# Kernel optimization log

Hardware: AMD Instinct MI355X
Metric: run time of the kernel (lower is better)

## Reference

```python
import jax, jax.numpy as jnp
import numpy as np

B, T, C, H, N = 2, 1024, 2048, 32, 64  # C == H*N, head_size fixed at 64
LAYER, NLAYERS = 12, 24
EPS = 1e-5 * 64.0  # GroupNorm eps = 1e-5 * 8**2


def _structured_params():
    r01 = LAYER / (NLAYERS - 1)          # ratio_0_to_1
    r1a0 = 1.0 - LAYER / NLAYERS         # ratio_1_to_almost0
    ddd = np.arange(C, dtype=np.float64) / C
    n = np.arange(C, dtype=np.float64)
    p = {}
    p['maa_x'] = 1.0 - ddd ** r1a0
    p['maa_w'] = 1.0 - ddd ** r1a0
    p['maa_k'] = 1.0 - ddd ** r1a0
    p['maa_v'] = 1.0 - (ddd ** r1a0 + 0.3 * r01)
    p['maa_r'] = 1.0 - ddd ** (0.5 * r1a0)
    p['maa_g'] = 1.0 - ddd ** (0.5 * r1a0)
    p['time_decay'] = -6.0 + 5.0 * (n / (C - 1)) ** (0.7 + 1.3 * r01)
    zig = ((n + 1) % 3 - 1) * 0.1
    p['u'] = (r01 * (1.0 - n / (C - 1)) + zig).reshape(H, N)  # time_faaaa
    return {k: jnp.asarray(v, jnp.float32) for k, v in p.items()}


def setup_inputs():
    key = jax.random.key(0)
    ks = jax.random.split(key, 12)
    inp = {'x': jax.random.normal(ks[0], (B, T, C), jnp.float32)}
    inp.update(_structured_params())
    inp['maa_w1'] = jax.random.uniform(ks[1], (C, 5 * 32), jnp.float32, -1e-4, 1e-4)
    inp['maa_w2'] = jax.random.uniform(ks[2], (5, 32, C), jnp.float32, -1e-4, 1e-4)
    inp['td_w1'] = jax.random.uniform(ks[3], (C, 64), jnp.float32, -1e-4, 1e-4)
    inp['td_w2'] = jax.random.uniform(ks[4], (64, C), jnp.float32, -1e-4, 1e-4)
    for i, name in enumerate(['Wr', 'Wk', 'Wv', 'Wg', 'Wo']):
        inp[name] = jax.random.normal(ks[5 + i], (C, C), jnp.float32) * 0.02  # applied as x @ W
    inp['ln_g'] = jnp.ones((C,), jnp.float32)
    inp['ln_b'] = jnp.zeros((C,), jnp.float32)
    return inp


def _wkv6(r, k, v, w, u):
    # r,k,v,w: [B,T,C]; u: [H,N].  y_t = r_t . (u*k_t v_t^T + S_t); S_{t+1} = exp(-exp(w_t))*S_t + k_t v_t^T
    def heads(a):
        return a.reshape(B, T, H, N).transpose(1, 0, 2, 3)  # [T,B,H,N]
    r, k, v = heads(r), heads(k), heads(v)
    d = jnp.exp(-jnp.exp(heads(w)))  # data-dependent per-channel decay

    def step(S, inp):
        r_t, k_t, v_t, d_t = inp  # each [B,H,N]
        y = jnp.einsum('bhj,bhji->bhi', r_t, S) \
            + jnp.sum(r_t * u * k_t, axis=-1, keepdims=True) * v_t
        S = d_t[..., None] * S + k_t[..., None] * v_t[..., None, :]
        return S, y

    S0 = jnp.zeros((B, H, N, N), jnp.float32)
    _, y = jax.lax.scan(step, S0, (r, k, v, d))
    return y.transpose(1, 0, 2, 3).reshape(B, T, C)


def reference(x, maa_x, maa_w, maa_k, maa_v, maa_r, maa_g, time_decay, u,
              maa_w1, maa_w2, td_w1, td_w2, Wr, Wk, Wv, Wg, Wo, ln_g, ln_b):
    # token shift: ZeroPad2d((0,0,1,-1)) == shift right by one along T with zero at t=0
    xx = jnp.pad(x, ((0, 0), (1, 0), (0, 0)))[:, :-1] - x
    xxx = x + xx * maa_x
    m = jnp.tanh(xxx @ maa_w1).reshape(B, T, 5, 32)
    m = jnp.einsum('btfd,fdc->fbtc', m, maa_w2)  # [5,B,T,C]
    mw, mk, mv, mr, mg = m[0], m[1], m[2], m[3], m[4]
    xw = x + xx * (maa_w + mw)
    xk = x + xx * (maa_k + mk)
    xv = x + xx * (maa_v + mv)
    xr = x + xx * (maa_r + mr)
    xg = x + xx * (maa_g + mg)
    r = xr @ Wr
    k = xk @ Wk
    v = xv @ Wv
    g = jax.nn.silu(xg @ Wg)
    w = time_decay + jnp.tanh(xw @ td_w1) @ td_w2  # [B,T,C]

    y = _wkv6(r, k, v, w, u)

    # GroupNorm(H groups over C), applied per (b,t) row
    yh = y.reshape(B, T, H, N)
    mu = yh.mean(-1, keepdims=True)
    var = yh.var(-1, keepdims=True)
    yn = (yh - mu) * jax.lax.rsqrt(var + EPS)
    yn = yn * ln_g.reshape(H, N) + ln_b.reshape(H, N)
    y = yn.reshape(B, T, C)
    return (y * g) @ Wo
```

## Files before the change

kernel.cpp:

```cpp
#include <hip/hip_runtime.h>
#include <cstdint>
#include <cstddef>

#define B_  2
#define T_  1024
#define C_  2048
#define H_  32
#define BT_ (B_*T_)
static constexpr float EPS_GN = 1e-5f * 64.0f;

using short8 = __attribute__((ext_vector_type(8))) short;
using f32x4  = __attribute__((ext_vector_type(4))) float;
typedef unsigned short bfu16;

__device__ __forceinline__ bfu16 f2b(float f) {
  uint32_t x = __float_as_uint(f);
  uint32_t r = (x + 0x7FFFu + ((x >> 16) & 1u)) >> 16;
  return (bfu16)r;
}
__device__ __forceinline__ float b2f(bfu16 h) {
  return __uint_as_float(((uint32_t)h) << 16);
}

__device__ __forceinline__ void gload16(const bfu16* g, bfu16* l) {
  __builtin_amdgcn_global_load_lds((__attribute__((address_space(1))) void*)g,
                                   (__attribute__((address_space(3))) void*)l,
                                   16, 0, 0);
}

struct G256P {
  const bfu16* Bt; float* of;
  size_t bStr, oStr;
  int ldk, nkt, kSplit;
  const bfu16* aArr[4];
};

__global__ __launch_bounds__(512, 2)
void gemm256(G256P p)
{
  extern __shared__ __align__(16) bfu16 sm[];
  const int tid  = threadIdx.x;
  const int nwg = gridDim.x * gridDim.y * gridDim.z;
  int lin = blockIdx.x + gridDim.x * (blockIdx.y + gridDim.y * blockIdx.z);
  lin = (lin & 7) * (nwg >> 3) + (lin >> 3);
  const int bx = lin % gridDim.x;
  const int by = (lin / gridDim.x) % gridDim.y;
  const int z  = lin / (gridDim.x * gridDim.y);
  const int m0   = by * 256, n0 = bx * 256;
  const int lane = tid & 63;
  const int wv   = tid >> 6;
  const int wm   = wv >> 2, wn = wv & 3;
  const int ldk  = p.ldk;

  const bfu16* A;
  size_t koff;
  if (p.kSplit > 1) { A = p.aArr[0]; koff = (size_t)z * p.nkt * 64; }
  else              { A = p.aArr[z]; koff = 0; }
  const bfu16* Bt = p.Bt + (size_t)z * p.bStr;

  const int srow = tid >> 3;
  const int scol = (tid & 7) * 8;
  const int sswz = (srow & 7) << 3;
  const bfu16* gA = A  + (size_t)(m0 + srow) * ldk + koff + (scol ^ sswz);
  const bfu16* gB = Bt + (size_t)(n0 + srow) * ldk + koff + (scol ^ sswz);

  auto STAGE_A = [&](bfu16* dst, int kt) {
    const bfu16* g = gA + (size_t)kt * 64;
    bfu16* l = dst + srow * 64 + scol;
#pragma unroll
    for (int it = 0; it < 4; ++it)
      gload16(g + (size_t)it * 64 * ldk, l + it * 4096);
  };
  auto STAGE_B = [&](bfu16* dst, int kt) {
    const bfu16* g = gB + (size_t)kt * 64;
    bfu16* l = dst + srow * 64 + scol;
#pragma unroll
    for (int it = 0; it < 4; ++it)
      gload16(g + (size_t)it * 64 * ldk, l + it * 4096);
  };

  f32x4 acc[8][4];
  const f32x4 zero = {0.f, 0.f, 0.f, 0.f};
#pragma unroll
  for (int i = 0; i < 8; ++i)
#pragma unroll
    for (int j = 0; j < 4; ++j) acc[i][j] = zero;

  STAGE_A(sm, 0);
  STAGE_B(sm + 32768, 0);

  const int rswz = (lane & 7) << 3;

  for (int kt = 0; kt < p.nkt; ++kt) {
    bfu16* curA = sm + (kt & 1) * 16384;
    bfu16* curB = sm + 32768 + (kt & 1) * 16384;
    bfu16* nxtA = sm + ((kt & 1) ^ 1) * 16384;
    bfu16* nxtB = sm + 32768 + ((kt & 1) ^ 1) * 16384;
    const bool more = (kt + 1 < p.nkt);
    if (more) {
      STAGE_A(nxtA, kt + 1);
      asm volatile("s_waitcnt vmcnt(4)" ::: "memory");
    } else {
      asm volatile("s_waitcnt vmcnt(0)" ::: "memory");
    }
    __builtin_amdgcn_s_barrier();

#pragma unroll
    for (int ks = 0; ks < 2; ++ks) {
      if (ks == 1 && more) STAGE_B(nxtB, kt + 1);
      const int ko = (ks * 32 + (lane >> 4) * 8) ^ rswz;
      short8 a[8], b[4];
#pragma unroll
      for (int i = 0; i < 8; ++i)
        a[i] = *(const short8*)(curA + (wm * 128 + i * 16 + (lane & 15)) * 64 + ko);
#pragma unroll
      for (int j = 0; j < 4; ++j)
        b[j] = *(const short8*)(curB + (wn * 64 + j * 16 + (lane & 15)) * 64 + ko);
      __builtin_amdgcn_s_setprio(1);
#pragma unroll
      for (int i = 0; i < 8; ++i)
#pragma unroll
        for (int j = 0; j < 4; ++j)
          acc[i][j] = __builtin_amdgcn_mfma_f32_16x16x32_bf16(a[i], b[j], acc[i][j], 0, 0, 0);
      __builtin_amdgcn_s_setprio(0);
    }
    __builtin_amdgcn_s_barrier();
  }

  float* o = p.of + (size_t)z * p.oStr;
  const int cb = n0 + wn * 64 + (lane & 15);
  const int rb = m0 + wm * 128 + ((lane >> 4) << 2);
#pragma unroll
  for (int i = 0; i < 8; ++i)
#pragma unroll
    for (int j = 0; j < 4; ++j) {
      int col = cb + j * 16;
#pragma unroll
      for (int q = 0; q < 4; ++q)
        o[(size_t)(rb + i * 16 + q) * 2048 + col] = acc[i][j][q];
    }
}

struct GemmP {
  const bfu16* A; const bfu16* Bt;
  float* of; bfu16* ob;
  const bfu16* xh; const bfu16* xxh;
  int ldk, kIters, kChunk, ldo;
  size_t pStride, aStr, bStr, oStr;
  const float* vArr[5];
};

template<int MODE>
__global__ __launch_bounds__(256)
void gemm_k(GemmP p)
{
  __shared__ alignas(16) bfu16 As[128*64];
  __shared__ alignas(16) bfu16 Bs[128*64];
  const int tid  = threadIdx.x;
  const int z    = blockIdx.z;
  const int m0   = blockIdx.y * 128, n0 = blockIdx.x * 128;
  const int lane = tid & 63;
  const int wv   = tid >> 6;
  const int wr   = (wv >> 1) * 64, wc = (wv & 1) * 64;

  const bfu16* A  = p.A;
  const bfu16* Bt = p.Bt;
  size_t koff = 0;
  if constexpr (MODE == 7) { A += (size_t)z * p.aStr; Bt += (size_t)z * p.bStr; }
  if constexpr (MODE == 5) { koff = (size_t)z * p.kChunk; }

  f32x4 acc[4][4];
  const f32x4 zero = {0.f, 0.f, 0.f, 0.f};
#pragma unroll
  for (int i = 0; i < 4; ++i)
#pragma unroll
    for (int j = 0; j < 4; ++j) acc[i][j] = zero;

  const int srow = tid >> 3;
  const int scol = (tid & 7) * 8;
  const int ldk  = p.ldk;

  for (int kb = 0; kb < p.kIters; ++kb) {
    const bfu16* ga = A  + (size_t)m0 * ldk + koff + kb * 64;
    const bfu16* gb = Bt + (size_t)n0 * ldk + koff + kb * 64;
#pragma unroll
    for (int it = 0; it < 4; ++it) {
      int r = it * 32 + srow;
      gload16(ga + (size_t)r * ldk + scol, As + r * 64 + scol);
      gload16(gb + (size_t)r * ldk + scol, Bs + r * 64 + scol);
    }
    __syncthreads();
#pragma unroll
    for (int kk = 0; kk < 2; ++kk) {
      const int ko = kk * 32 + (lane >> 4) * 8;
      short8 a[4], b[4];
#pragma unroll
      for (int i = 0; i < 4; ++i)
        a[i] = *(const short8*)(As + (wr + i * 16 + (lane & 15)) * 64 + ko);
#pragma unroll
      for (int j = 0; j < 4; ++j)
        b[j] = *(const short8*)(Bs + (wc + j * 16 + (lane & 15)) * 64 + ko);
#pragma unroll
      for (int i = 0; i < 4; ++i)
#pragma unroll
        for (int j = 0; j < 4; ++j)
          acc[i][j] = __builtin_amdgcn_mfma_f32_16x16x32_bf16(a[i], b[j], acc[i][j], 0, 0, 0);
    }
    __syncthreads();
  }

  const int cb = n0 + wc + (lane & 15);
  const int rb = m0 + wr + ((lane >> 4) << 2);
#pragma unroll
  for (int i = 0; i < 4; ++i) {
#pragma unroll
    for (int j = 0; j < 4; ++j) {
      int col = cb + j * 16;
#pragma unroll
      for (int q = 0; q < 4; ++q) {
        int row = rb + i * 16 + q;
        float v = acc[i][j][q];
        if constexpr (MODE == 4) {
          p.of[(size_t)row * p.ldo + col] = -__expf(p.vArr[0][col] + v);
        } else if constexpr (MODE == 5) {
          p.of[(size_t)z * p.pStride + (size_t)row * p.ldo + col] = v;
        } else if constexpr (MODE == 7) {
          size_t idx = (size_t)row * C_ + col;
          (p.ob + (size_t)z * p.oStr)[idx] =
              f2b(b2f(p.xh[idx]) + b2f(p.xxh[idx]) * (p.vArr[z][col] + v));
        }
      }
    }
  }
}

template<int OUT>
__global__ __launch_bounds__(256)
void redk_tanh(const float* __restrict__ part, size_t pStr, int ldo, int ncols,
               bfu16* __restrict__ out)
{
  int id = blockIdx.x * 256 + threadIdx.x;
  int row = id / ncols, col = id % ncols;
  if (row >= BT_) return;
  float v = 0.f;
#pragma unroll
  for (int s = 0; s < 8; ++s) v += part[(size_t)s * pStr + (size_t)row * ldo + col];
  bfu16 tv = f2b(tanhf(v));
  if constexpr (OUT == 0)
    out[((size_t)(col >> 5) * BT_ + row) * 64 + (col & 31)] = tv;
  else
    out[(size_t)row * 64 + col] = tv;
}

__global__ __launch_bounds__(256)
void redk_sum4(const float* __restrict__ p0, float* __restrict__ out)
{
  size_t i = ((size_t)blockIdx.x * 256 + threadIdx.x) * 4;
  const size_t str = (size_t)2048 * 2048;
  float4 a = *(const float4*)(p0 + i);
  float4 b = *(const float4*)(p0 + str + i);
  float4 c = *(const float4*)(p0 + 2 * str + i);
  float4 d = *(const float4*)(p0 + 3 * str + i);
  a.x += b.x + c.x + d.x; a.y += b.y + c.y + d.y;
  a.z += b.z + c.z + d.z; a.w += b.w + c.w + d.w;
  *(float4*)(out + i) = a;
}

struct TrP { const float* src[5]; bfu16* dst; size_t dStr; int R, Cc, Rpad, ldd; };

__global__ __launch_bounds__(256)
void transpose_k(TrP p)
{
  __shared__ float tile[32][33];
  const float* src = p.src[blockIdx.z];
  bfu16* dst = p.dst + (size_t)blockIdx.z * p.dStr;
  const int tx = threadIdx.x & 31, ty = threadIdx.x >> 5;
  const int r0 = blockIdx.y * 32, c0 = blockIdx.x * 32;
#pragma unroll
  for (int i = 0; i < 4; ++i) {
    int r = r0 + ty + i * 8, c = c0 + tx;
    tile[ty + i * 8][tx] = (r < p.R && c < p.Cc) ? src[(size_t)r * p.Cc + c] : 0.f;
  }
  __syncthreads();
#pragma unroll
  for (int i = 0; i < 4; ++i) {
    int c = c0 + ty + i * 8, r = r0 + tx;
    if (c < p.Cc && r < p.Rpad) dst[(size_t)c * p.ldd + r] = f2b(tile[tx][ty + i * 8]);
  }
}

__global__ __launch_bounds__(256)
void prep_xx(const float* __restrict__ x, const float* __restrict__ maa_x,
             bfu16* __restrict__ xxh, bfu16* __restrict__ xxx,
             bfu16* __restrict__ xh)
{
  size_t i = ((size_t)blockIdx.x * 256 + threadIdx.x) * 4;
  int c  = (int)(i & (C_ - 1));
  int bt = (int)(i >> 11);
  int t  = bt & (T_ - 1);
  float4 xv = *(const float4*)(x + i);
  float4 xp = {0.f, 0.f, 0.f, 0.f};
  if (t > 0) xp = *(const float4*)(x + i - C_);
  float4 mx = *(const float4*)(maa_x + c);
  float dx = xp.x - xv.x, dy = xp.y - xv.y, dz = xp.z - xv.z, dw = xp.w - xv.w;
  uint2 w0;
  w0.x = (uint32_t)f2b(dx) | ((uint32_t)f2b(dy) << 16);
  w0.y = (uint32_t)f2b(dz) | ((uint32_t)f2b(dw) << 16);
  *(uint2*)(xxh + i) = w0;
  uint2 w1;
  w1.x = (uint32_t)f2b(xv.x + dx * mx.x) | ((uint32_t)f2b(xv.y + dy * mx.y) << 16);
  w1.y = (uint32_t)f2b(xv.z + dz * mx.z) | ((uint32_t)f2b(xv.w + dw * mx.w) << 16);
  *(uint2*)(xxx + i) = w1;
  uint2 w2;
  w2.x = (uint32_t)f2b(xv.x) | ((uint32_t)f2b(xv.y) << 16);
  w2.y = (uint32_t)f2b(xv.z) | ((uint32_t)f2b(xv.w) << 16);
  *(uint2*)(xh + i) = w2;
}

#define STR 76

__global__ __launch_bounds__(256)
void wkv_a(const float* __restrict__ r, const float* __restrict__ k,
           const float* __restrict__ v, const float* __restrict__ w,
           const float* __restrict__ u, float* __restrict__ rp,
           float* __restrict__ y, float* __restrict__ U, float* __restrict__ G)
{
  __shared__ float rw[64 * STR];
  __shared__ float kk[64 * STR];
  __shared__ float vv[64 * STR];
  __shared__ float Ps[64 * STR];
  __shared__ float red[4][64];
  __shared__ float diag[64];
  __shared__ float Gl[64];

  const int blk = blockIdx.x;
  const int bh = blk >> 4, c = blk & 15;
  const int b = bh >> 5, h = bh & 31;
  const int tid = threadIdx.x;
  const size_t gbase = ((size_t)(b * T_ + c * 64)) * C_ + h * 64;

  {
    const int t = tid >> 2, q = tid & 3;
    const size_t g = gbase + (size_t)t * C_ + q * 16;
    const int l = t * STR + q * 16;
#pragma unroll
    for (int p = 0; p < 4; ++p) {
      *(float4*)(rw + l + p * 4) = *(const float4*)(r + g + p * 4);
      *(float4*)(kk + l + p * 4) = *(const float4*)(k + g + p * 4);
      *(float4*)(vv + l + p * 4) = *(const float4*)(v + g + p * 4);
      *(float4*)(Ps + l + p * 4) = *(const float4*)(w + g + p * 4);
    }
  }
  __syncthreads();

  {
    const int seg = tid >> 6, j = tid & 63;
    float loc = 0.f;
#pragma unroll
    for (int tt = 0; tt < 16; ++tt) loc += Ps[(seg * 16 + tt) * STR + j];
    red[seg][j] = loc;
  }
  __syncthreads();
  {
    const int seg = tid >> 6, j = tid & 63;
    float cs = 0.f;
    for (int s = 0; s < seg; ++s) cs += red[s][j];
    const float uj = u[h * 64 + j];
#pragma unroll
    for (int tt = 0; tt < 16; ++tt) {
      const int a = (seg * 16 + tt) * STR + j;
      float lw = Ps[a];
      float rv = rw[a] * __expf(cs);
      rw[a] = rv;
      cs += lw;
      float kv = kk[a] * __expf(-cs);
      kk[a] = kv;
      Ps[a] = rv * kv * uj * __expf(lw);
    }
    if (seg == 3) {
      float Gj = __expf(cs);
      Gl[j] = Gj;
      G[((size_t)bh * 16 + c) * 64 + j] = Gj;
    }
  }
  __syncthreads();

  {
    const int t = tid & 63, q = tid >> 6;
    float s = 0.f;
#pragma unroll
    for (int jj = 0; jj < 16; ++jj) s += Ps[t * STR + q * 16 + jj];
    red[q][t] = s;
  }
  __syncthreads();
  if (tid < 64) diag[tid] = red[0][tid] + red[1][tid] + red[2][tid] + red[3][tid];
  __syncthreads();

  {
    const int tq = tid >> 4, sq = tid & 15;
    float acc[4][4] = {{0.f}};
    if (sq <= tq) {
      for (int j = 0; j < 64; j += 4) {
        float4 a0 = *(const float4*)(rw + (tq * 4 + 0) * STR + j);
        float4 a1 = *(const float4*)(rw + (tq * 4 + 1) * STR + j);
        float4 a2 = *(const float4*)(rw + (tq * 4 + 2) * STR + j);
        float4 a3 = *(const float4*)(rw + (tq * 4 + 3) * STR + j);
        float4 b0 = *(const float4*)(kk + (sq * 4 + 0) * STR + j);
        float4 b1 = *(const float4*)(kk + (sq * 4 + 1) * STR + j);
        float4 b2 = *(const float4*)(kk + (sq * 4 + 2) * STR + j);
        float4 b3 = *(const float4*)(kk + (sq * 4 + 3) * STR + j);
        const float4 av[4] = {a0, a1, a2, a3};
        const float4 bv[4] = {b0, b1, b2, b3};
#pragma unroll
        for (int tt = 0; tt < 4; ++tt)
#pragma unroll
          for (int ss = 0; ss < 4; ++ss)
            acc[tt][ss] += av[tt].x * bv[ss].x + av[tt].y * bv[ss].y
                         + av[tt].z * bv[ss].z + av[tt].w * bv[ss].w;
      }
    }
#pragma unroll
    for (int tt = 0; tt < 4; ++tt)
#pragma unroll
      for (int ss = 0; ss < 4; ++ss) {
        int t = tq * 4 + tt, s = sq * 4 + ss;
        Ps[t * STR + s] = (s < t) ? acc[tt][ss] : (s == t ? diag[t] : 0.f);
      }
  }
  __syncthreads();

  {
    const int tq = tid >> 4, iq = tid & 15;
    float o[4][4] = {{0.f}};
    for (int s4 = 0; s4 <= tq; ++s4) {
#pragma unroll
      for (int ss = 0; ss < 4; ++ss) {
        const int s = s4 * 4 + ss;
        float4 vx = *(const float4*)(vv + s * STR + iq * 4);
        float p0 = Ps[(tq * 4 + 0) * STR + s];
        float p1 = Ps[(tq * 4 + 1) * STR + s];
        float p2 = Ps[(tq * 4 + 2) * STR + s];
        float p3 = Ps[(tq * 4 + 3) * STR + s];
        o[0][0] += p0 * vx.x; o[0][1] += p0 * vx.y; o[0][2] += p0 * vx.z; o[0][3] += p0 * vx.w;
        o[1][0] += p1 * vx.x; o[1][1] += p1 * vx.y; o[1][2] += p1 * vx.z; o[1][3] += p1 * vx.w;
        o[2][0] += p2 * vx.x; o[2][1] += p2 * vx.y; o[2][2] += p2 * vx.z; o[2][3] += p2 * vx.w;
        o[3][0] += p3 * vx.x; o[3][1] += p3 * vx.y; o[3][2] += p3 * vx.z; o[3][3] += p3 * vx.w;
      }
    }
#pragma unroll
    for (int tt = 0; tt < 4; ++tt) {
      float4 ov = {o[tt][0], o[tt][1], o[tt][2], o[tt][3]};
      *(float4*)(y + gbase + (size_t)(tq * 4 + tt) * C_ + iq * 4) = ov;
    }
  }

  {
    const int jq = tid >> 4, iq = tid & 15;
    float ua[4][4] = {{0.f}};
    for (int s = 0; s < 64; ++s) {
      float4 kx = *(const float4*)(kk + s * STR + jq * 4);
      float4 vx = *(const float4*)(vv + s * STR + iq * 4);
      ua[0][0] += kx.x * vx.x; ua[0][1] += kx.x * vx.y; ua[0][2] += kx.x * vx.z; ua[0][3] += kx.x * vx.w;
      ua[1][0] += kx.y * vx.x; ua[1][1] += kx.y * vx.y; ua[1][2] += kx.y * vx.z; ua[1][3] += kx.y * vx.w;
      ua[2][0] += kx.z * vx.x; ua[2][1] += kx.z * vx.y; ua[2][2] += kx.z * vx.z; ua[2][3] += kx.z * vx.w;
      ua[3][0] += kx.w * vx.x; ua[3][1] += kx.w * vx.y; ua[3][2] += kx.w * vx.z; ua[3][3] += kx.w * vx.w;
    }
    const size_t ub = ((size_t)bh * 16 + c) * 4096;
#pragma unroll
    for (int jj = 0; jj < 4; ++jj) {
      float g = Gl[jq * 4 + jj];
      float4 uv = {ua[jj][0] * g, ua[jj][1] * g, ua[jj][2] * g, ua[jj][3] * g};
      *(float4*)(U + ub + (size_t)(jq * 4 + jj) * 64 + iq * 4) = uv;
    }
  }

  {
    const int t = tid >> 2, q = tid & 3;
#pragma unroll
    for (int p = 0; p < 4; ++p)
      *(float4*)(rp + gbase + (size_t)t * C_ + q * 16 + p * 4) =
          *(const float4*)(rw + t * STR + q * 16 + p * 4);
  }
}

__global__ __launch_bounds__(256)
void wkv_b(const float* __restrict__ U, const float* __restrict__ G,
           float* __restrict__ Sbuf)
{
  const int bh = blockIdx.x;
  const int tid = threadIdx.x;
  const int i = tid & 63, jq = tid >> 6;
  __shared__ float Gl[64];
  float S[16];
#pragma unroll
  for (int jj = 0; jj < 16; ++jj) S[jj] = 0.f;
  for (int c = 0; c < 16; ++c) {
    if (tid < 64) Gl[tid] = G[((size_t)bh * 16 + c) * 64 + tid];
    __syncthreads();
    const size_t base = ((size_t)bh * 16 + c) * 4096;
#pragma unroll
    for (int jj = 0; jj < 16; ++jj) {
      const int j = jq * 16 + jj;
      Sbuf[base + (size_t)j * 64 + i] = S[jj];
      S[jj] = Gl[j] * S[jj] + U[base + (size_t)j * 64 + i];
    }
    __syncthreads();
  }
}

__global__ __launch_bounds__(256)
void wkv_c(const float* __restrict__ rp, const float* __restrict__ Sbuf,
           float* __restrict__ y)
{
  __shared__ float Sl[64 * 68];
  __shared__ float rl[64 * 68];
  const int blk = blockIdx.x;
  const int bh = blk >> 4, c = blk & 15;
  const int b = bh >> 5, h = bh & 31;
  const int tid = threadIdx.x;
  const size_t gbase = ((size_t)(b * T_ + c * 64)) * C_ + h * 64;
  {
    const int t = tid >> 2, q = tid & 3;
    const size_t sb = ((size_t)bh * 16 + c) * 4096 + (size_t)t * 64 + q * 16;
    const size_t gr = gbase + (size_t)t * C_ + q * 16;
    const int l = t * 68 + q * 16;
#pragma unroll
    for (int p = 0; p < 4; ++p) {
      *(float4*)(rl + l + p * 4) = *(const float4*)(rp + gr + p * 4);
      *(float4*)(Sl + l + p * 4) = *(const float4*)(Sbuf + sb + p * 4);
    }
  }
  __syncthreads();
  const int tq = tid >> 4, iq = tid & 15;
  float o[4][4] = {{0.f}};
  for (int j = 0; j < 64; ++j) {
    float4 sv = *(const float4*)(Sl + j * 68 + iq * 4);
    float r0 = rl[(tq * 4 + 0) * 68 + j];
    float r1 = rl[(tq * 4 + 1) * 68 + j];
    float r2 = rl[(tq * 4 + 2) * 68 + j];
    float r3 = rl[(tq * 4 + 3) * 68 + j];
    o[0][0] += r0 * sv.x; o[0][1] += r0 * sv.y; o[0][2] += r0 * sv.z; o[0][3] += r0 * sv.w;
    o[1][0] += r1 * sv.x; o[1][1] += r1 * sv.y; o[1][2] += r1 * sv.z; o[1][3] += r1 * sv.w;
    o[2][0] += r2 * sv.x; o[2][1] += r2 * sv.y; o[2][2] += r2 * sv.z; o[2][3] += r2 * sv.w;
    o[3][0] += r3 * sv.x; o[3][1] += r3 * sv.y; o[3][2] += r3 * sv.z; o[3][3] += r3 * sv.w;
  }
#pragma unroll
  for (int tt = 0; tt < 4; ++tt) {
    float* yp = y + gbase + (size_t)(tq * 4 + tt) * C_ + iq * 4;
    float4 yv = *(const float4*)yp;
    yv.x += o[tt][0]; yv.y += o[tt][1]; yv.z += o[tt][2]; yv.w += o[tt][3];
    *(float4*)yp = yv;
  }
}

__global__ __launch_bounds__(256)
void gnorm_kernel(const float* __restrict__ y, const float* __restrict__ gpre,
                  const float* __restrict__ lng, const float* __restrict__ lnb,
                  bfu16* __restrict__ yg)
{
  const int bt = blockIdx.x;
  const int wv = threadIdx.x >> 6, lane = threadIdx.x & 63;
#pragma unroll
  for (int it = 0; it < 8; ++it) {
    int hh = it * 4 + wv;
    int c = hh * 64 + lane;
    size_t idx = (size_t)bt * C_ + c;
    float yv = y[idx];
    float s = yv, sq = yv * yv;
#pragma unroll
    for (int m = 1; m < 64; m <<= 1) {
      s  += __shfl_xor(s, m, 64);
      sq += __shfl_xor(sq, m, 64);
    }
    float mu  = s * (1.f / 64.f);
    float var = sq * (1.f / 64.f) - mu * mu;
    float yn  = (yv - mu) * rsqrtf(var + EPS_GN);
    yn = yn * lng[c] + lnb[c];
    float gp = gpre[idx];
    float gs = gp / (1.f + __expf(-gp));
    yg[idx] = f2b(yn * gs);
  }
}

extern "C" void kernel_launch(void* const* d_in, const int* in_sizes, int n_in,
                              void* d_out, int out_size, void* d_ws, size_t ws_size,
                              hipStream_t stream)
{
  const float* x      = (const float*)d_in[0];
  const float* maa_x  = (const float*)d_in[1];
  const float* maa_w  = (const float*)d_in[2];
  const float* maa_k  = (const float*)d_in[3];
  const float* maa_v  = (const float*)d_in[4];
  const float* maa_r  = (const float*)d_in[5];
  const float* maa_g  = (const float*)d_in[6];
  const float* tdec   = (const float*)d_in[7];
  const float* u      = (const float*)d_in[8];
  const float* maa_w1 = (const float*)d_in[9];
  const float* maa_w2 = (const float*)d_in[10];
  const float* td_w1  = (const float*)d_in[11];
  const float* td_w2  = (const float*)d_in[12];
  const float* lng = (const float*)d_in[18];
  const float* lnb = (const float*)d_in[19];
  float* out = (float*)d_out;

  char* wsp = (char*)d_ws;
  auto alloc = [&](size_t bytes) -> char* {
    char* p = wsp;
    wsp += (bytes + 255) & ~(size_t)255;
    return p;
  };

  bfu16* WT0 = (bfu16*)alloc((size_t)5 * 2048 * 2048 * 2);
  bfu16* w1T  = (bfu16*)alloc((size_t)256 * 2048 * 2);
  bfu16* tw1T = (bfu16*)alloc((size_t)128 * 2048 * 2);
  bfu16* tw2T = (bfu16*)alloc((size_t)2048 * 64 * 2);
  bfu16* w2T  = (bfu16*)alloc((size_t)5 * 2048 * 64 * 2);
  float* ybuf = (float*)alloc((size_t)BT_ * C_ * 4);
  bfu16* xxh  = (bfu16*)alloc((size_t)BT_ * C_ * 2);
  bfu16* xxx  = (bfu16*)alloc((size_t)BT_ * C_ * 2);
  bfu16* xh   = (bfu16*)alloc((size_t)BT_ * C_ * 2);
  bfu16* mtan = (bfu16*)alloc((size_t)5 * BT_ * 64 * 2);
  bfu16* xmix0 = (bfu16*)alloc((size_t)5 * BT_ * C_ * 2);
  float* rbuf = (float*)alloc((size_t)4 * BT_ * C_ * 4);
  float* kbuf = rbuf + (size_t)BT_ * C_;
  float* vbuf = kbuf + (size_t)BT_ * C_;
  float* gbuf = vbuf + (size_t)BT_ * C_;
  float* wbuf = (float*)alloc((size_t)BT_ * C_ * 4);
  bfu16* wtan = (bfu16*)alloc((size_t)BT_ * 64 * 2);
  bfu16* ygb  = xxx;
  float* Ubuf = (float*)(xmix0 + (size_t)1 * BT_ * C_);
  float* Sbuf = (float*)(xmix0 + (size_t)3 * BT_ * C_);
  float* Gbuf = (float*)wtan;
  float* part1 = rbuf;
  float* part3 = wbuf;
  float* partW = rbuf;

  hipMemsetAsync(mtan, 0, (size_t)5 * BT_ * 64 * 2, stream);

  dim3 tb(256);

  {
    TrP p{}; for (int i = 0; i < 5; ++i) p.src[i] = (const float*)d_in[13 + i];
    p.dst = WT0; p.dStr = (size_t)2048 * 2048; p.R = 2048; p.Cc = 2048; p.Rpad = 2048; p.ldd = 2048;
    transpose_k<<<dim3(64, 64, 5), tb, 0, stream>>>(p);
  }
  {
    TrP p{}; p.src[0] = maa_w1; p.dst = w1T; p.dStr = 0;
    p.R = 2048; p.Cc = 160; p.Rpad = 2048; p.ldd = 2048;
    transpose_k<<<dim3(5, 64, 1), tb, 0, stream>>>(p);
  }
  {
    TrP p{}; p.src[0] = td_w1; p.dst = tw1T; p.dStr = 0;
    p.R = 2048; p.Cc = 64; p.Rpad = 2048; p.ldd = 2048;
    transpose_k<<<dim3(2, 64, 1), tb, 0, stream>>>(p);
  }
  {
    TrP p{}; p.src[0] = td_w2; p.dst = tw2T; p.dStr = 0;
    p.R = 64; p.Cc = 2048; p.Rpad = 64; p.ldd = 64;
    transpose_k<<<dim3(64, 2, 1), tb, 0, stream>>>(p);
  }
  {
    TrP p{}; for (int f = 0; f < 5; ++f) p.src[f] = maa_w2 + (size_t)f * 32 * 2048;
    p.dst = w2T; p.dStr = (size_t)2048 * 64;
    p.R = 32; p.Cc = 2048; p.Rpad = 64; p.ldd = 64;
    transpose_k<<<dim3(64, 2, 5), tb, 0, stream>>>(p);
  }

  prep_xx<<<dim3((BT_ * C_ / 4) / 256), tb, 0, stream>>>(x, maa_x, xxh, xxx, xh);

  {
    GemmP p{}; p.A = xxx; p.Bt = w1T; p.ldk = 2048; p.kIters = 4; p.kChunk = 256;
    p.ldo = 256; p.pStride = (size_t)BT_ * 256; p.of = part1;
    gemm_k<5><<<dim3(2, 16, 8), tb, 0, stream>>>(p);
  }
  redk_tanh<0><<<dim3(BT_ * 160 / 256), tb, 0, stream>>>(part1, (size_t)BT_ * 256, 256, 160, mtan);

  {
    GemmP p{}; p.A = mtan; p.Bt = w2T; p.ldk = 64; p.kIters = 1;
    p.aStr = (size_t)BT_ * 64; p.bStr = (size_t)2048 * 64; p.oStr = (size_t)BT_ * C_;
    p.ob = xmix0; p.xh = xh; p.xxh = xxh;
    p.vArr[0] = maa_w; p.vArr[1] = maa_k; p.vArr[2] = maa_v; p.vArr[3] = maa_r; p.vArr[4] = maa_g;
    gemm_k<7><<<dim3(16, 16, 5), tb, 0, stream>>>(p);
  }

  {
    G256P p{}; p.Bt = WT0; p.ldk = 2048; p.nkt = 32; p.kSplit = 1;
    p.bStr = (size_t)2048 * 2048; p.oStr = (size_t)BT_ * C_; p.of = rbuf;
    p.aArr[0] = xmix0 + (size_t)3 * BT_ * C_;
    p.aArr[1] = xmix0 + (size_t)1 * BT_ * C_;
    p.aArr[2] = xmix0 + (size_t)2 * BT_ * C_;
    p.aArr[3] = xmix0 + (size_t)4 * BT_ * C_;
    gemm256<<<dim3(8, 8, 4), dim3(512), 131072, stream>>>(p);
  }

  {
    GemmP p{}; p.A = xmix0; p.Bt = tw1T; p.ldk = 2048; p.kIters = 4; p.kChunk = 256;
    p.ldo = 128; p.pStride = (size_t)BT_ * 128; p.of = part3;
    gemm_k<5><<<dim3(1, 16, 8), tb, 0, stream>>>(p);
  }
  redk_tanh<1><<<dim3(BT_ * 64 / 256), tb, 0, stream>>>(part3, (size_t)BT_ * 128, 128, 64, wtan);

  {
    GemmP p{}; p.A = wtan; p.Bt = tw2T; p.ldk = 64; p.kIters = 1;
    p.of = wbuf; p.ldo = 2048; p.vArr[0] = tdec;
    gemm_k<4><<<dim3(16, 16, 1), tb, 0, stream>>>(p);
  }

  wkv_a<<<dim3(1024), tb, 0, stream>>>(rbuf, kbuf, vbuf, wbuf, u, rbuf, ybuf, Ubuf, Gbuf);
  wkv_b<<<dim3(64),   tb, 0, stream>>>(Ubuf, Gbuf, Sbuf);
  wkv_c<<<dim3(1024), tb, 0, stream>>>(rbuf, Sbuf, ybuf);

  gnorm_kernel<<<dim3(BT_), tb, 0, stream>>>(ybuf, gbuf, lng, lnb, ygb);

  {
    G256P p{}; p.Bt = WT0 + (size_t)4 * 2048 * 2048; p.ldk = 2048;
    p.nkt = 8; p.kSplit = 4;
    p.bStr = 0; p.oStr = (size_t)2048 * 2048; p.of = partW;
    p.aArr[0] = ygb;
    gemm256<<<dim3(8, 8, 4), dim3(512), 131072, stream>>>(p);
  }
  redk_sum4<<<dim3(4096), tb, 0, stream>>>(partW, out);
}
```

Baseline: 338.2 us.

## Halve WKV chunk length to 32 and issue GEMM B-tile prefetch earlier

Reworks the chunked WKV kernels to use 32-token chunks instead of 64. This doubles the block count and shrinks the per-block intra-chunk quadratic work and shared memory, at the cost of a longer sequential state scan in wkv_b and more state buffers. The state and decay buffers move to dedicated allocations sized for the larger chunk count. Separately, the GEMM main loop now stages the next B tile together with the A tile before the barrier, waiting on vmcnt(8) instead of issuing B mid-compute.

```diff
diff --git a/kernel.cpp b/kernel.cpp
--- a/kernel.cpp
+++ b/kernel.cpp
@@ -99,7 +99,8 @@
     const bool more = (kt + 1 < p.nkt);
     if (more) {
       STAGE_A(nxtA, kt + 1);
-      asm volatile("s_waitcnt vmcnt(4)" ::: "memory");
+      STAGE_B(nxtB, kt + 1);
+      asm volatile("s_waitcnt vmcnt(8)" ::: "memory");
     } else {
       asm volatile("s_waitcnt vmcnt(0)" ::: "memory");
     }
@@ -107,7 +108,6 @@
 
 #pragma unroll
     for (int ks = 0; ks < 2; ++ks) {
-      if (ks == 1 && more) STAGE_B(nxtB, kt + 1);
       const int ko = (ks * 32 + (lane >> 4) * 8) ^ rswz;
       short8 a[8], b[4];
 #pragma unroll
@@ -317,39 +317,40 @@
   *(uint2*)(xh + i) = w2;
 }
 
-#define STR 76
-
-__global__ __launch_bounds__(256)
-void wkv_a(const float* __restrict__ r, const float* __restrict__ k,
-           const float* __restrict__ v, const float* __restrict__ w,
-           const float* __restrict__ u, float* __restrict__ rp,
-           float* __restrict__ y, float* __restrict__ U, float* __restrict__ G)
-{
-  __shared__ float rw[64 * STR];
-  __shared__ float kk[64 * STR];
-  __shared__ float vv[64 * STR];
-  __shared__ float Ps[64 * STR];
-  __shared__ float red[4][64];
-  __shared__ float diag[64];
+#define S32 68
+
+__global__ __launch_bounds__(256)
+void wkv_a32(const float* __restrict__ r, const float* __restrict__ k,
+             const float* __restrict__ v, const float* __restrict__ w,
+             const float* __restrict__ u, float* __restrict__ rp,
+             float* __restrict__ y, float* __restrict__ U, float* __restrict__ G)
+{
+  __shared__ float rw[32 * S32];
+  __shared__ float kk[32 * S32];
+  __shared__ float vv[32 * S32];
+  __shared__ float Ps[32 * S32];
+  __shared__ float red[256];
+  __shared__ float diag[32];
   __shared__ float Gl[64];
 
   const int blk = blockIdx.x;
-  const int bh = blk >> 4, c = blk & 15;
+  const int bh = blk >> 5, c = blk & 31;
   const int b = bh >> 5, h = bh & 31;
   const int tid = threadIdx.x;
-  const size_t gbase = ((size_t)(b * T_ + c * 64)) * C_ + h * 64;
-
-  {
-    const int t = tid >> 2, q = tid & 3;
-    const size_t g = gbase + (size_t)t * C_ + q * 16;
-    const int l = t * STR + q * 16;
-#pragma unroll
-    for (int p = 0; p < 4; ++p) {
-      *(float4*)(rw + l + p * 4) = *(const float4*)(r + g + p * 4);
-      *(float4*)(kk + l + p * 4) = *(const float4*)(k + g + p * 4);
-      *(float4*)(vv + l + p * 4) = *(const float4*)(v + g + p * 4);
-      *(float4*)(Ps + l + p * 4) = *(const float4*)(w + g + p * 4);
-    }
+  const size_t gbase = ((size_t)(b * T_ + c * 32)) * C_ + h * 64;
+
+  {
+    const int t = tid >> 3, q = tid & 7;
+    const size_t g = gbase + (size_t)t * C_ + q * 8;
+    const int l = t * S32 + q * 8;
+    *(float4*)(rw + l)     = *(const float4*)(r + g);
+    *(float4*)(rw + l + 4) = *(const float4*)(r + g + 4);
+    *(float4*)(kk + l)     = *(const float4*)(k + g);
+    *(float4*)(kk + l + 4) = *(const float4*)(k + g + 4);
+    *(float4*)(vv + l)     = *(const float4*)(v + g);
+    *(float4*)(vv + l + 4) = *(const float4*)(v + g + 4);
+    *(float4*)(Ps + l)     = *(const float4*)(w + g);
+    *(float4*)(Ps + l + 4) = *(const float4*)(w + g + 4);
   }
   __syncthreads();
 
@@ -357,18 +358,18 @@
     const int seg = tid >> 6, j = tid & 63;
     float loc = 0.f;
 #pragma unroll
-    for (int tt = 0; tt < 16; ++tt) loc += Ps[(seg * 16 + tt) * STR + j];
-    red[seg][j] = loc;
+    for (int tt = 0; tt < 8; ++tt) loc += Ps[(seg * 8 + tt) * S32 + j];
+    red[seg * 64 + j] = loc;
   }
   __syncthreads();
   {
     const int seg = tid >> 6, j = tid & 63;
     float cs = 0.f;
-    for (int s = 0; s < seg; ++s) cs += red[s][j];
+    for (int s = 0; s < seg; ++s) cs += red[s * 64 + j];
     const float uj = u[h * 64 + j];
 #pragma unroll
-    for (int tt = 0; tt < 16; ++tt) {
-      const int a = (seg * 16 + tt) * STR + j;
+    for (int tt = 0; tt < 8; ++tt) {
+      const int a = (seg * 8 + tt) * S32 + j;
       float lw = Ps[a];
       float rv = rw[a] * __expf(cs);
       rw[a] = rv;
@@ -380,92 +381,85 @@
     if (seg == 3) {
       float Gj = __expf(cs);
       Gl[j] = Gj;
-      G[((size_t)bh * 16 + c) * 64 + j] = Gj;
+      G[((size_t)bh * 32 + c) * 64 + j] = Gj;
     }
   }
   __syncthreads();
 
   {
-    const int t = tid & 63, q = tid >> 6;
+    const int t = tid & 31, q = tid >> 5;
     float s = 0.f;
 #pragma unroll
-    for (int jj = 0; jj < 16; ++jj) s += Ps[t * STR + q * 16 + jj];
-    red[q][t] = s;
+    for (int jj = 0; jj < 8; ++jj) s += Ps[t * S32 + q * 8 + jj];
+    red[q * 32 + t] = s;
   }
   __syncthreads();
-  if (tid < 64) diag[tid] = red[0][tid] + red[1][tid] + red[2][tid] + red[3][tid];
+  if (tid < 32) {
+    float d = 0.f;
+#pragma unroll
+    for (int q = 0; q < 8; ++q) d += red[q * 32 + tid];
+    diag[tid] = d;
+  }
   __syncthreads();
 
   {
     const int tq = tid >> 4, sq = tid & 15;
-    float acc[4][4] = {{0.f}};
+    float a00 = 0.f, a01 = 0.f, a10 = 0.f, a11 = 0.f;
     if (sq <= tq) {
       for (int j = 0; j < 64; j += 4) {
-        float4 a0 = *(const float4*)(rw + (tq * 4 + 0) * STR + j);
-        float4 a1 = *(const float4*)(rw + (tq * 4 + 1) * STR + j);
-        float4 a2 = *(const float4*)(rw + (tq * 4 + 2) * STR + j);
-        float4 a3 = *(const float4*)(rw + (tq * 4 + 3) * STR + j);
-        float4 b0 = *(const float4*)(kk + (sq * 4 + 0) * STR + j);
-        float4 b1 = *(const float4*)(kk + (sq * 4 + 1) * STR + j);
-        float4 b2 = *(const float4*)(kk + (sq * 4 + 2) * STR + j);
-        float4 b3 = *(const float4*)(kk + (sq * 4 + 3) * STR + j);
-        const float4 av[4] = {a0, a1, a2, a3};
-        const float4 bv[4] = {b0, b1, b2, b3};
-#pragma unroll
-        for (int tt = 0; tt < 4; ++tt)
-#pragma unroll
-          for (int ss = 0; ss < 4; ++ss)
-            acc[tt][ss] += av[tt].x * bv[ss].x + av[tt].y * bv[ss].y
-                         + av[tt].z * bv[ss].z + av[tt].w * bv[ss].w;
+        float4 r0 = *(const float4*)(rw + (2 * tq + 0) * S32 + j);
+        float4 r1 = *(const float4*)(rw + (2 * tq + 1) * S32 + j);
+        float4 k0 = *(const float4*)(kk + (2 * sq + 0) * S32 + j);
+        float4 k1 = *(const float4*)(kk + (2 * sq + 1) * S32 + j);
+        a00 += r0.x * k0.x + r0.y * k0.y + r0.z * k0.z + r0.w * k0.w;
+        a01 += r0.x * k1.x + r0.y * k1.y + r0.z * k1.z + r0.w * k1.w;
+        a10 += r1.x * k0.x + r1.y * k0.y + r1.z * k0.z + r1.w * k0.w;
+        a11 += r1.x * k1.x + r1.y * k1.y + r1.z * k1.z + r1.w * k1.w;
       }
     }
-#pragma unroll
-    for (int tt = 0; tt < 4; ++tt)
-#pragma unroll
-      for (int ss = 0; ss < 4; ++ss) {
-        int t = tq * 4 + tt, s = sq * 4 + ss;
-        Ps[t * STR + s] = (s < t) ? acc[tt][ss] : (s == t ? diag[t] : 0.f);
-      }
+    __syncthreads();
+    if (sq <= tq) {
+      const float av[2][2] = {{a00, a01}, {a10, a11}};
+#pragma unroll
+      for (int tt = 0; tt < 2; ++tt)
+#pragma unroll
+        for (int ss = 0; ss < 2; ++ss) {
+          int t = 2 * tq + tt, s = 2 * sq + ss;
+          Ps[t * S32 + s] = (s < t) ? av[tt][ss] : (s == t ? diag[t] : 0.f);
+        }
+    }
   }
   __syncthreads();
 
   {
     const int tq = tid >> 4, iq = tid & 15;
-    float o[4][4] = {{0.f}};
-    for (int s4 = 0; s4 <= tq; ++s4) {
-#pragma unroll
-      for (int ss = 0; ss < 4; ++ss) {
-        const int s = s4 * 4 + ss;
-        float4 vx = *(const float4*)(vv + s * STR + iq * 4);
-        float p0 = Ps[(tq * 4 + 0) * STR + s];
-        float p1 = Ps[(tq * 4 + 1) * STR + s];
-        float p2 = Ps[(tq * 4 + 2) * STR + s];
-        float p3 = Ps[(tq * 4 + 3) * STR + s];
-        o[0][0] += p0 * vx.x; o[0][1] += p0 * vx.y; o[0][2] += p0 * vx.z; o[0][3] += p0 * vx.w;
-        o[1][0] += p1 * vx.x; o[1][1] += p1 * vx.y; o[1][2] += p1 * vx.z; o[1][3] += p1 * vx.w;
-        o[2][0] += p2 * vx.x; o[2][1] += p2 * vx.y; o[2][2] += p2 * vx.z; o[2][3] += p2 * vx.w;
-        o[3][0] += p3 * vx.x; o[3][1] += p3 * vx.y; o[3][2] += p3 * vx.z; o[3][3] += p3 * vx.w;
-      }
-    }
-#pragma unroll
-    for (int tt = 0; tt < 4; ++tt) {
-      float4 ov = {o[tt][0], o[tt][1], o[tt][2], o[tt][3]};
-      *(float4*)(y + gbase + (size_t)(tq * 4 + tt) * C_ + iq * 4) = ov;
-    }
+    float o0[4] = {0.f, 0.f, 0.f, 0.f}, o1[4] = {0.f, 0.f, 0.f, 0.f};
+    const int tmax = 2 * tq + 1;
+    for (int s = 0; s <= tmax; ++s) {
+      float4 vx = *(const float4*)(vv + s * S32 + iq * 4);
+      float p0 = Ps[(2 * tq + 0) * S32 + s];
+      float p1 = Ps[(2 * tq + 1) * S32 + s];
+      o0[0] += p0 * vx.x; o0[1] += p0 * vx.y; o0[2] += p0 * vx.z; o0[3] += p0 * vx.w;
+      o1[0] += p1 * vx.x; o1[1] += p1 * vx.y; o1[2] += p1 * vx.z; o1[3] += p1 * vx.w;
+    }
+    float4 w0 = {o0[0], o0[1], o0[2], o0[3]};
+    float4 w1 = {o1[0], o1[1], o1[2], o1[3]};
+    *(float4*)(y + gbase + (size_t)(2 * tq + 0) * C_ + iq * 4) = w0;
+    *(float4*)(y + gbase + (size_t)(2 * tq + 1) * C_ + iq * 4) = w1;
   }
 
   {
     const int jq = tid >> 4, iq = tid & 15;
     float ua[4][4] = {{0.f}};
-    for (int s = 0; s < 64; ++s) {
-      float4 kx = *(const float4*)(kk + s * STR + jq * 4);
-      float4 vx = *(const float4*)(vv + s * STR + iq * 4);
+    for (int s = 0; s < 32; ++s) {
+      float4 kx = *(const float4*)(kk + s * S32 + jq * 4);
+      float4 vx = *(const float4*)(vv + s * S32 + iq * 4);
       ua[0][0] += kx.x * vx.x; ua[0][1] += kx.x * vx.y; ua[0][2] += kx.x * vx.z; ua[0][3] += kx.x * vx.w;
       ua[1][0] += kx.y * vx.x; ua[1][1] += kx.y * vx.y; ua[1][2] += kx.y * vx.z; ua[1][3] += kx.y * vx.w;
       ua[2][0] += kx.z * vx.x; ua[2][1] += kx.z * vx.y; ua[2][2] += kx.z * vx.z; ua[2][3] += kx.z * vx.w;
       ua[3][0] += kx.w * vx.x; ua[3][1] += kx.w * vx.y; ua[3][2] += kx.w * vx.z; ua[3][3] += kx.w * vx.w;
     }
-    const size_t ub = ((size_t)bh * 16 + c) * 4096;
+    const size_t ub = ((size_t)bh * 32 + c) * 4096;
 #pragma unroll
     for (int jj = 0; jj < 4; ++jj) {
       float g = Gl[jq * 4 + jj];
@@ -475,17 +469,17 @@
   }
 
   {
-    const int t = tid >> 2, q = tid & 3;
-#pragma unroll
-    for (int p = 0; p < 4; ++p)
-      *(float4*)(rp + gbase + (size_t)t * C_ + q * 16 + p * 4) =
-          *(const float4*)(rw + t * STR + q * 16 + p * 4);
-  }
-}
-
-__global__ __launch_bounds__(256)
-void wkv_b(const float* __restrict__ U, const float* __restrict__ G,
-           float* __restrict__ Sbuf)
+    const int t = tid >> 3, q = tid & 7;
+    const size_t g = gbase + (size_t)t * C_ + q * 8;
+    const int l = t * S32 + q * 8;
+    *(float4*)(rp + g)     = *(const float4*)(rw + l);
+    *(float4*)(rp + g + 4) = *(const float4*)(rw + l + 4);
+  }
+}
+
+__global__ __launch_bounds__(256)
+void wkv_b32(const float* __restrict__ U, const float* __restrict__ G,
+             float* __restrict__ Sbuf)
 {
   const int bh = blockIdx.x;
   const int tid = threadIdx.x;
@@ -494,10 +488,10 @@
   float S[16];
 #pragma unroll
   for (int jj = 0; jj < 16; ++jj) S[jj] = 0.f;
-  for (int c = 0; c < 16; ++c) {
-    if (tid < 64) Gl[tid] = G[((size_t)bh * 16 + c) * 64 + tid];
+  for (int c = 0; c < 32; ++c) {
+    if (tid < 64) Gl[tid] = G[((size_t)bh * 32 + c) * 64 + tid];
     __syncthreads();
-    const size_t base = ((size_t)bh * 16 + c) * 4096;
+    const size_t base = ((size_t)bh * 32 + c) * 4096;
 #pragma unroll
     for (int jj = 0; jj < 16; ++jj) {
       const int j = jq * 16 + jj;
@@ -509,46 +503,47 @@
 }
 
 __global__ __launch_bounds__(256)
-void wkv_c(const float* __restrict__ rp, const float* __restrict__ Sbuf,
-           float* __restrict__ y)
-{
-  __shared__ float Sl[64 * 68];
-  __shared__ float rl[64 * 68];
+void wkv_c32(const float* __restrict__ rp, const float* __restrict__ Sbuf,
+             float* __restrict__ y)
+{
+  __shared__ float Sl[64 * S32];
+  __shared__ float rl[32 * S32];
   const int blk = blockIdx.x;
-  const int bh = blk >> 4, c = blk & 15;
+  const int bh = blk >> 5, c = blk & 31;
   const int b = bh >> 5, h = bh & 31;
   const int tid = threadIdx.x;
-  const size_t gbase = ((size_t)(b * T_ + c * 64)) * C_ + h * 64;
-  {
-    const int t = tid >> 2, q = tid & 3;
-    const size_t sb = ((size_t)bh * 16 + c) * 4096 + (size_t)t * 64 + q * 16;
-    const size_t gr = gbase + (size_t)t * C_ + q * 16;
-    const int l = t * 68 + q * 16;
-#pragma unroll
-    for (int p = 0; p < 4; ++p) {
-      *(float4*)(rl + l + p * 4) = *(const float4*)(rp + gr + p * 4);
+  const size_t gbase = ((size_t)(b * T_ + c * 32)) * C_ + h * 64;
+  {
+    const int j = tid >> 2, q = tid & 3;
+    const size_t sb = ((size_t)bh * 32 + c) * 4096 + (size_t)j * 64 + q * 16;
+    const int l = j * S32 + q * 16;
+#pragma unroll
+    for (int p = 0; p < 4; ++p)
       *(float4*)(Sl + l + p * 4) = *(const float4*)(Sbuf + sb + p * 4);
-    }
+    const int t = tid >> 3, q8 = tid & 7;
+    const size_t gr = gbase + (size_t)t * C_ + q8 * 8;
+    const int lr = t * S32 + q8 * 8;
+    *(float4*)(rl + lr)     = *(const float4*)(rp + gr);
+    *(float4*)(rl + lr + 4) = *(const float4*)(rp + gr + 4);
   }
   __syncthreads();
   const int tq = tid >> 4, iq = tid & 15;
-  float o[4][4] = {{0.f}};
+  float o0[4] = {0.f, 0.f, 0.f, 0.f}, o1[4] = {0.f, 0.f, 0.f, 0.f};
   for (int j = 0; j < 64; ++j) {
-    float4 sv = *(const float4*)(Sl + j * 68 + iq * 4);
-    float r0 = rl[(tq * 4 + 0) * 68 + j];
-    float r1 = rl[(tq * 4 + 1) * 68 + j];
-    float r2 = rl[(tq * 4 + 2) * 68 + j];
-    float r3 = rl[(tq * 4 + 3) * 68 + j];
-    o[0][0] += r0 * sv.x; o[0][1] += r0 * sv.y; o[0][2] += r0 * sv.z; o[0][3] += r0 * sv.w;
-    o[1][0] += r1 * sv.x; o[1][1] += r1 * sv.y; o[1][2] += r1 * sv.z; o[1][3] += r1 * sv.w;
-    o[2][0] += r2 * sv.x; o[2][1] += r2 * sv.y; o[2][2] += r2 * sv.z; o[2][3] += r2 * sv.w;
-    o[3][0] += r3 * sv.x; o[3][1] += r3 * sv.y; o[3][2] += r3 * sv.z; o[3][3] += r3 * sv.w;
-  }
-#pragma unroll
-  for (int tt = 0; tt < 4; ++tt) {
-    float* yp = y + gbase + (size_t)(tq * 4 + tt) * C_ + iq * 4;
+    float4 sv = *(const float4*)(Sl + j * S32 + iq * 4);
+    float r0 = rl[(2 * tq + 0) * S32 + j];
+    float r1 = rl[(2 * tq + 1) * S32 + j];
+    o0[0] += r0 * sv.x; o0[1] += r0 * sv.y; o0[2] += r0 * sv.z; o0[3] += r0 * sv.w;
+    o1[0] += r1 * sv.x; o1[1] += r1 * sv.y; o1[2] += r1 * sv.z; o1[3] += r1 * sv.w;
+  }
+  {
+    float* yp = y + gbase + (size_t)(2 * tq + 0) * C_ + iq * 4;
     float4 yv = *(const float4*)yp;
-    yv.x += o[tt][0]; yv.y += o[tt][1]; yv.z += o[tt][2]; yv.w += o[tt][3];
+    yv.x += o0[0]; yv.y += o0[1]; yv.z += o0[2]; yv.w += o0[3];
+    *(float4*)yp = yv;
+    yp = y + gbase + (size_t)(2 * tq + 1) * C_ + iq * 4;
+    yv = *(const float4*)yp;
+    yv.x += o1[0]; yv.y += o1[1]; yv.z += o1[2]; yv.w += o1[3];
     *(float4*)yp = yv;
   }
 }
@@ -627,10 +622,10 @@
   float* gbuf = vbuf + (size_t)BT_ * C_;
   float* wbuf = (float*)alloc((size_t)BT_ * C_ * 4);
   bfu16* wtan = (bfu16*)alloc((size_t)BT_ * 64 * 2);
+  float* Sbuf = (float*)alloc((size_t)64 * 32 * 4096 * 4);
+  float* Gbuf = (float*)alloc((size_t)64 * 32 * 64 * 4);
   bfu16* ygb  = xxx;
   float* Ubuf = (float*)(xmix0 + (size_t)1 * BT_ * C_);
-  float* Sbuf = (float*)(xmix0 + (size_t)3 * BT_ * C_);
-  float* Gbuf = (float*)wtan;
   float* part1 = rbuf;
   float* part3 = wbuf;
   float* partW = rbuf;
@@ -706,9 +701,9 @@
     gemm_k<4><<<dim3(16, 16, 1), tb, 0, stream>>>(p);
   }
 
-  wkv_a<<<dim3(1024), tb, 0, stream>>>(rbuf, kbuf, vbuf, wbuf, u, rbuf, ybuf, Ubuf, Gbuf);
-  wkv_b<<<dim3(64),   tb, 0, stream>>>(Ubuf, Gbuf, Sbuf);
-  wkv_c<<<dim3(1024), tb, 0, stream>>>(rbuf, Sbuf, ybuf);
+  wkv_a32<<<dim3(2048), tb, 0, stream>>>(rbuf, kbuf, vbuf, wbuf, u, rbuf, ybuf, Ubuf, Gbuf);
+  wkv_b32<<<dim3(64),   tb, 0, stream>>>(Ubuf, Gbuf, Sbuf);
+  wkv_c32<<<dim3(2048), tb, 0, stream>>>(rbuf, Sbuf, ybuf);
 
   gnorm_kernel<<<dim3(BT_), tb, 0, stream>>>(ybuf, gbuf, lng, lnb, ygb);
 
```

New measurement: 347.8 us. 1.03x slower.
